# Optimization experiments

Hardware: AMD Instinct MI355X
Metric: run time of the kernel (lower is better)

The kernel has to match this reference:

```python
import jax, jax.numpy as jnp
import numpy as np
from jax import lax

B, T_IN, N, C_IN = 64, 12, 716, 2
RC = DC = 32      # residual / dilation channels
SC = 8            # skip channels
EC = 512          # end channels
OUT = 12
DIMS = 40
DAYS = 288
TOD = 288
TOPK = 100
DILS = [1, 2, 1, 2, 1, 2, 1, 2]  # blocks=4, layers=2
L = len(DILS)


def setup_inputs() -> dict:
    key = jax.random.key(0)
    ks = iter(jax.random.split(key, 64))
    n = lambda shape, s=0.1: jax.random.normal(next(ks), shape, jnp.float32) * s
    return dict(
        history_data=jax.random.uniform(next(ks), (B, T_IN, N, C_IN), jnp.float32),
        alpha=jnp.float32(-5.0),
        nodevec_p1=n((DAYS, DIMS), 1.0),
        nodevec_p2=n((N, DIMS), 1.0),
        nodevec_p3=n((N, DIMS), 1.0),
        nodevec_pk=n((DIMS, DIMS, DIMS), 1.0),
        pivweight=n((N, N), 1.0),
        start_W=n((RC, 1)), start_b=n((RC,)),
        starta_W=n((1, 1)), starta_b=n((1,)),
        filter_W=n((L, DC, RC, 1, 2)), filter_b=n((L, DC)),
        gate_W=n((L, DC, RC, 1, 2)), gate_b=n((L, DC)),
        skip_W=n((L, SC, DC)), skip_b=n((L, SC)),
        gconv_W=n((L, RC, 3 * DC)), gconv_b=n((L, RC)),
        pgconv_W=n((L, RC, 3 * RC)), pgconv_b=n((L, RC)),
        bn_gamma=jnp.ones((L, RC), jnp.float32),
        bn_beta=jnp.zeros((L, RC), jnp.float32),
        end1_W=n((EC, SC * 52)), end1_b=n((EC,)),
        end2_W=n((OUT, EC)), end2_b=n((OUT,)),
    )


def _conv1x1(x, W, b):  # x [B,C,N,T], W [O,C]
    return jnp.einsum('bcnt,oc->bont', x, W) + b[None, :, None, None]


def _gcn(x, A, W, b):
    # diffusion order 2 over one support; A [B,N,N] or [N,N]
    sub = 'bcvt,bwv->bcwt' if A.ndim == 3 else 'bcvt,wv->bcwt'
    x1 = jnp.einsum(sub, x, A)
    x2 = jnp.einsum(sub, x1, A)
    return _conv1x1(jnp.concatenate([x, x1, x2], axis=1), W, b)


def _forward(history_data, alpha, nodevec_p1, nodevec_p2, nodevec_p3, nodevec_pk,
             pivweight, start_W, start_b, starta_W, starta_b,
             filter_W, filter_b, gate_W, gate_b, skip_W, skip_b,
             gconv_W, gconv_b, pgconv_W, pgconv_b, bn_gamma, bn_beta,
             end1_W, end1_b, end2_W, end2_b):
    inputs = jnp.transpose(history_data[..., 0:1], (0, 3, 2, 1))  # [B,1,N,T]
    inputs = jnp.pad(inputs, ((0, 0), (0, 0), (0, 0), (1, 0)))    # T -> 13 = receptive field
    ind = (history_data[:, -1, 0, 1] * TOD).astype(jnp.int32) % DAYS

    x = _conv1x1(inputs, start_W, start_b)      # [B,RC,N,13]
    x_a = _conv1x1(inputs, starta_W, starta_b)  # [B,1,N,13]

    # dynamic adjacency (dgconstruct)
    adp = jnp.einsum('ai,ijk->ajk', nodevec_p1[ind], nodevec_pk)
    adp = jnp.einsum('bj,ajk->abk', nodevec_p2, adp)
    adp = jnp.einsum('ck,abk->abc', nodevec_p3, adp)
    adj = jax.nn.softmax(jax.nn.relu(adp), axis=2)  # [B,N,N]

    # pivotal adjacency (pivotalconstruct) with top-k node mask
    xs = x_a[:, 0].sum(0)                   # [N,T]
    y = xs.sum(1)[None, :]                  # [1,N]
    adjp = (xs[:, :-1] @ xs[:, 1:].T) / y   # [N,N]
    adjp = adjp * pivweight
    score = adjp.sum(0) + adjp.sum(1)
    _, idx = lax.top_k(score, TOPK)
    mask = jnp.zeros((N,), bool).at[idx].set(True)
    adj_p = jax.nn.softmax(jax.nn.relu(adjp * mask[:, None] * mask[None, :]), axis=1)  # [N,N]

    a_s = jax.nn.sigmoid(alpha)
    dn = ('NCHW', 'OIHW', 'NCHW')
    skip = None
    for i, d in enumerate(DILS):
        residual = x
        filt = jnp.tanh(
            lax.conv_general_dilated(residual, filter_W[i], (1, 1), 'VALID',
                                     rhs_dilation=(1, d), dimension_numbers=dn)
            + filter_b[i][None, :, None, None])
        gate = jax.nn.sigmoid(
            lax.conv_general_dilated(residual, gate_W[i], (1, 1), 'VALID',
                                     rhs_dilation=(1, d), dimension_numbers=dn)
            + gate_b[i][None, :, None, None])
        xg = _gcn(filt * gate, adj, gconv_W[i], gconv_b[i])  # [B,RC,N,T-d]
        # pgcn: diffusion on residual, then causal temporal crop by dilation
        xa = _gcn(residual, adj_p, pgconv_W[i], pgconv_b[i])[..., : residual.shape[3] - d]
        x = a_s * xa + (1.0 - a_s) * xg
        x = x + residual[..., -x.shape[3]:]
        s = _conv1x1(x, skip_W[i], skip_b[i])  # [B,SC,N,Ti]
        s = jnp.transpose(s, (0, 1, 3, 2)).reshape(s.shape[0], -1, s.shape[2], 1)  # [B,SC*Ti,N,1]
        skip = s if skip is None else jnp.concatenate([s, skip], axis=1)
        # BatchNorm2d, train-mode batch stats, fresh affine
        mu = x.mean(axis=(0, 2, 3), keepdims=True)
        var = x.var(axis=(0, 2, 3), keepdims=True)
        x = ((x - mu) / jnp.sqrt(var + 1e-5)) * bn_gamma[i][None, :, None, None] \
            + bn_beta[i][None, :, None, None]

    out = jax.nn.relu(skip)                         # [B,SC*52,N,1]
    out = jax.nn.relu(_conv1x1(out, end1_W, end1_b))
    out = _conv1x1(out, end2_W, end2_b)             # [B,OUT,N,1]
    return out


def reference(history_data, alpha, nodevec_p1, nodevec_p2, nodevec_p3, nodevec_pk,
              pivweight, start_W, start_b, starta_W, starta_b,
              filter_W, filter_b, gate_W, gate_b, skip_W, skip_b,
              gconv_W, gconv_b, pgconv_W, pgconv_b, bn_gamma, bn_beta,
              end1_W, end1_b, end2_W, end2_b):
    return _forward(history_data, alpha, nodevec_p1, nodevec_p2, nodevec_p3, nodevec_pk,
                    pivweight, start_W, start_b, starta_W, starta_b,
                    filter_W, filter_b, gate_W, gate_b, skip_W, skip_b,
                    gconv_W, gconv_b, pgconv_W, pgconv_b, bn_gamma, bn_beta,
                    end1_W, end1_b, end2_W, end2_b)
```

## Files before the change

### kernel.cpp

```cpp
#include <hip/hip_runtime.h>
#include <math.h>

#define NN 716
#define NSQ (716*716)
#define MAXG 9216
#define FPAD 70
typedef unsigned short bfu;
typedef __attribute__((ext_vector_type(8))) __bf16 bf16x8;
typedef __attribute__((ext_vector_type(4))) float f32x4;

__device__ __forceinline__ float b2f(bfu u){ union{unsigned int i; float f;} x; x.i = ((unsigned int)u)<<16; return x.f; }
__device__ __forceinline__ bfu f2b(float f){ union{float fv; unsigned int i;} x; x.fv = f; unsigned int r = (x.i + 0x7fffu + ((x.i>>16)&1u)) >> 16; return (bfu)r; }
__device__ __forceinline__ float sigmoidf_(float x){ return 1.f/(1.f+expf(-x)); }

__device__ __forceinline__ float fexp_(float x){
#if __has_builtin(__builtin_amdgcn_exp2f)
  return __builtin_amdgcn_exp2f(x * 1.44269504088896340736f);
#else
  return __expf(x);
#endif
}
__device__ __forceinline__ float frcp_(float x){
#if __has_builtin(__builtin_amdgcn_rcpf)
  return __builtin_amdgcn_rcpf(x);
#else
  return 1.f/x;
#endif
}
__device__ __forceinline__ float fsig_(float x){ return frcp_(1.f + fexp_(-x)); }
__device__ __forceinline__ float ftanh_(float x){
  float xc = fminf(fmaxf(x, -30.f), 30.f);
  float e = fexp_(-2.f*xc);
  return (1.f - e) * frcp_(1.f + e);
}


__global__ void k_ind(const float* __restrict__ hist, int* __restrict__ ind){
  int b = threadIdx.x; if (b >= 64) return;
  float v = hist[((b*12+11)*NN + 0)*2 + 1];
  ind[b] = ((int)(v*288.0f)) % 288;
}

__global__ void k_dg1(const float* __restrict__ p1, const float* __restrict__ pk,
                      const int* __restrict__ ind, float* __restrict__ tmp1){
  int b = blockIdx.x;
  __shared__ float p1s[40];
  if (threadIdx.x < 40) p1s[threadIdx.x] = p1[ind[b]*40 + threadIdx.x];
  __syncthreads();
  for (int jk = threadIdx.x; jk < 1600; jk += 256){
    float acc = 0.f;
    for (int i = 0; i < 40; ++i) acc += p1s[i]*pk[i*1600 + jk];
    tmp1[b*1600 + jk] = acc;
  }
}

__global__ void k_dg2(const float* __restrict__ p2, const float* __restrict__ tmp1,
                      float* __restrict__ tmp2){
  int b = blockIdx.y;
  __shared__ float ts[1600];
  for (int i = threadIdx.x; i < 1600; i += 256) ts[i] = tmp1[b*1600+i];
  __syncthreads();
  int idx = blockIdx.x*256 + threadIdx.x;
  if (idx >= NN*40) return;
  int n = idx/40, k = idx%40;
  float acc = 0.f;
  for (int j = 0; j < 40; ++j) acc += p2[n*40+j]*ts[j*40+k];
  tmp2[(long)b*NN*40 + idx] = acc;
}

__global__ void k_p3t(const float* __restrict__ p3, float* __restrict__ p3t){
  int v = blockIdx.x*256 + threadIdx.x; if (v >= NN) return;
  for (int k = 0; k < 40; ++k) p3t[k*NN + v] = p3[v*40 + k];
}

__global__ __launch_bounds__(256) void k_adjrow4s(const float* __restrict__ p3t,
    const float* __restrict__ tmp2, unsigned int* __restrict__ topA,
    int* __restrict__ cntA)
{
  int b = blockIdx.y, w0 = blockIdx.x*4, tid = threadIdx.x;
  int wave = tid >> 6, lane = tid & 63;
  __shared__ float t2s[4][40];
  __shared__ float buf[4][720];
  __shared__ float wred[4][4];
  __shared__ float rstat[4];
  __shared__ int pc[4][12];
  for (int i = tid; i < 160; i += 256){
    int r = i/40, k = i%40; int w = w0 + r;
    t2s[r][k] = (w < NN) ? tmp2[((long)b*NN + w)*40 + k] : 0.f;
  }
  __syncthreads();
  float lmax[4] = {0,0,0,0};
  for (int q = 0; q < 3; ++q){
    int v = tid + q*256;
    if (v < NN){
      float a[4] = {0,0,0,0};
      #pragma unroll 8
      for (int k = 0; k < 40; ++k){
        float pv = p3t[k*NN + v];
        #pragma unroll
        for (int r = 0; r < 4; ++r) a[r] += t2s[r][k]*pv;
      }
      #pragma unroll
      for (int r = 0; r < 4; ++r){
        float val = fmaxf(a[r], 0.f);
        buf[r][v] = val;
        lmax[r] = fmaxf(lmax[r], val);
      }
    }
  }
  #pragma unroll
  for (int r = 0; r < 4; ++r){
    float m = lmax[r];
    for (int s = 32; s > 0; s >>= 1) m = fmaxf(m, __shfl_xor(m, s, 64));
    if (lane == 0) wred[r][wave] = m;
  }
  __syncthreads();
  if (tid < 4) rstat[tid] = fmaxf(fmaxf(wred[tid][0], wred[tid][1]), fmaxf(wred[tid][2], wred[tid][3]));
  __syncthreads();
  float lsum[4] = {0,0,0,0};
  for (int q = 0; q < 3; ++q){
    int v = tid + q*256;
    if (v < NN){
      #pragma unroll
      for (int r = 0; r < 4; ++r){
        float e = fexp_(buf[r][v] - rstat[r]);
        buf[r][v] = e;
        lsum[r] += e;
      }
    }
  }
  __syncthreads();
  #pragma unroll
  for (int r = 0; r < 4; ++r){
    float s = lsum[r];
    for (int k = 32; k > 0; k >>= 1) s += __shfl_xor(s, k, 64);
    if (lane == 0) wred[r][wave] = s;
  }
  __syncthreads();
  if (tid < 4) rstat[tid] = frcp_(wred[tid][0] + wred[tid][1] + wred[tid][2] + wred[tid][3]);
  __syncthreads();
  for (int q = 0; q < 3; ++q){
    int v = tid + q*256;
    #pragma unroll
    for (int r = 0; r < 4; ++r){
      float p = (v < NN) ? buf[r][v]*rstat[r] : 0.f;
      unsigned long long m = __ballot(p >= 1e-7f);
      if (lane == 0) pc[r][q*4+wave] = __popcll(m);
    }
  }
  __syncthreads();
  for (int q = 0; q < 3; ++q){
    int v = tid + q*256;
    #pragma unroll
    for (int r = 0; r < 4; ++r){
      float p = (v < NN) ? buf[r][v]*rstat[r] : 0.f;
      bool qual = (p >= 1e-7f);
      unsigned long long m = __ballot(qual);
      int w = w0 + r;
      if (qual && w < NN){
        int base = 0, me = q*4+wave;
        for (int s = 0; s < me; ++s) base += pc[r][s];
        unsigned long long below = (lane == 0) ? 0ull : (m << (64-lane) >> (64-lane));
        int pos = base + __popcll(below);
        if (pos < 16)
          topA[((long)b*NN + w)*16 + pos] = (((unsigned)v)<<16) | (unsigned)f2b(p);
      }
    }
  }
  __syncthreads();
  if (tid < 4){
    int w = w0 + tid;
    if (w < NN){
      int tot = 0;
      for (int s = 0; s < 12; ++s) tot += pc[tid][s];
      cntA[(long)b*NN + w] = (tot < 16) ? tot : 16;
    }
  }
}

__global__ __launch_bounds__(256) void k_zgather(const bfu* __restrict__ Xg,
    const unsigned int* __restrict__ topA, const int* __restrict__ cntA,
    bfu* __restrict__ Zg, int M, long sx, long sz)
{
  __shared__ bfu rows[4][720];
  int b = blockIdx.y;
  int tid = threadIdx.x, wave = tid >> 6, lane = tid & 63;
  int m = blockIdx.x*4 + wave;
  if (m < M){
    const bfu* xr = Xg + (long)b*sx + (long)m*NN;
    #pragma unroll
    for (int q = 0; q < 12; ++q){
      int v = lane + q*64;
      if (v < NN) rows[wave][v] = xr[v];
    }
  }
  __syncthreads();
  if (m >= M) return;
  bfu* zr = Zg + (long)b*sz + (long)m*NN;
  const unsigned int* ta = topA + (long)b*NN*16;
  const int* ca = cntA + (long)b*NN;
  #pragma unroll
  for (int q = 0; q < 12; ++q){
    int w = lane + q*64;
    if (w < NN){
      int cnt = ca[w];
      const unsigned int* lst = ta + (long)w*16;
      float acc = 0.f;
      for (int j = 0; j < cnt; ++j){
        unsigned int e = lst[j];
        acc += b2f((bfu)(e & 0xffffu)) * b2f(rows[wave][e >> 16]);
      }
      zr[w] = f2b(acc);
    }
  }
}

__global__ void k_xs(const float* __restrict__ hist, const float* __restrict__ saW,
                     const float* __restrict__ sab, float* __restrict__ xs, float* __restrict__ y){
  int n = blockIdx.x, b = threadIdx.x;
  float w = saW[0], bb = sab[0];
  float ytot = 0.f;
  for (int t = 0; t < 13; ++t){
    float inp = (t == 0) ? 0.f : hist[((b*12 + (t-1))*NN + n)*2];
    float s = inp;
    for (int off = 32; off > 0; off >>= 1) s += __shfl_down(s, off, 64);
    if (b == 0){ float val = w*s + 64.f*bb; xs[n*13+t] = val; ytot += val; }
  }
  if (b == 0) y[n] = ytot;
}

__global__ void k_adjp(const float* __restrict__ xs, const float* __restrict__ y,
                       const float* __restrict__ piv, float* __restrict__ adjp){
  int i = blockIdx.y;
  __shared__ float xi[13];
  if (threadIdx.x < 13) xi[threadIdx.x] = xs[i*13+threadIdx.x];
  __syncthreads();
  int j = blockIdx.x*256 + threadIdx.x;
  if (j >= NN) return;
  float acc = 0.f;
  #pragma unroll
  for (int t = 0; t < 12; ++t) acc += xi[t]*xs[j*13+t+1];
  adjp[(long)i*NN+j] = acc / y[j] * piv[(long)i*NN+j];
}

__global__ void k_score(const float* __restrict__ adjp, float* __restrict__ score){
  int n = blockIdx.x, tid = threadIdx.x;
  float s = 0.f;
  for (int i = tid; i < NN; i += 256) s += adjp[(long)i*NN+n] + adjp[(long)n*NN+i];
  __shared__ float red[256];
  red[tid] = s; __syncthreads();
  for (int k = 128; k > 0; k >>= 1){ if (tid < k) red[tid] += red[tid+k]; __syncthreads(); }
  if (tid == 0) score[n] = red[0];
}

__global__ void k_topk(const float* __restrict__ score, int* __restrict__ mask){
  __shared__ float v[1024];
  __shared__ int ix[1024];
  int tid = threadIdx.x;
  for (int t = tid; t < 1024; t += 256){ v[t] = (t < NN) ? score[t] : -INFINITY; ix[t] = t; }
  __syncthreads();
  for (int k = 2; k <= 1024; k <<= 1){
    for (int j = k >> 1; j > 0; j >>= 1){
      for (int t = tid; t < 1024; t += 256){
        int l = t ^ j;
        if (l > t){
          bool up = ((t & k) == 0);
          bool g = (v[t] > v[l]) || (v[t] == v[l] && ix[t] < ix[l]);
          if (up ? !g : g){
            float tv = v[t]; v[t] = v[l]; v[l] = tv;
            int ti = ix[t]; ix[t] = ix[l]; ix[l] = ti;
          }
        }
      }
      __syncthreads();
    }
  }
  for (int t = tid; t < NN; t += 256) mask[t] = 0;
  __syncthreads();
  if (tid < 100) mask[ix[tid]] = 1;
}

__global__ void k_pivprep(const float* __restrict__ adjp, const int* __restrict__ mask,
                          int* __restrict__ idxk, int* __restrict__ rankv,
                          float* __restrict__ uvec, float* __restrict__ ApkT){
  __shared__ int sidx[100];
  int tid = threadIdx.x;
  if (tid == 0){
    int c = 0;
    for (int i = 0; i < NN; ++i){
      if (mask[i] && c < 100){ sidx[c] = i; idxk[c] = i; rankv[i] = c; ++c; }
      else rankv[i] = -1;
    }
  }
  __syncthreads();
  if (tid < 100){
    int i = sidx[tid];
    const float* row = adjp + (long)i*NN;
    float mx = 0.f;
    for (int k = 0; k < 100; ++k) mx = fmaxf(mx, row[sidx[k]]);
    float sum = 616.f * fexp_(-mx);
    for (int k = 0; k < 100; ++k) sum += fexp_(fmaxf(row[sidx[k]], 0.f) - mx);
    float inv = 1.f/sum;
    uvec[tid] = fexp_(-mx)*inv;
    for (int k = 0; k < 100; ++k)
      ApkT[k*100 + tid] = fexp_(fmaxf(row[sidx[k]], 0.f) - mx)*inv;
  }
}

__global__ void k_init_x(const float* __restrict__ hist, const float* __restrict__ sW,
                         const float* __restrict__ sb, bfu* __restrict__ x){
  int n = blockIdx.x*256 + threadIdx.x; if (n >= NN) return;
  int t = blockIdx.y, b = blockIdx.z;
  float inp = (t == 0) ? 0.f : hist[((b*12 + (t-1))*NN + n)*2];
  #pragma unroll
  for (int c = 0; c < 32; ++c)
    x[((long)(b*32+c)*13 + t)*NN + n] = f2b(sW[c]*inp + sb[c]);
}

__global__ void k_bnid(float* __restrict__ bnp){
  int c = threadIdx.x; if (c >= 32) return;
  bnp[c*2] = 1.f; bnp[c*2+1] = 0.f;
}

__global__ void k_bnfold(const float* __restrict__ fW, const float* __restrict__ fb,
                         const float* __restrict__ gW, const float* __restrict__ gb,
                         const float* __restrict__ bnp, bfu* __restrict__ Wcat,
                         float* __restrict__ bcat){
  int tid = threadIdx.x;
  for (int i = tid; i < 4096; i += 256){
    int row = i >> 6, k = i & 63;
    int o = row >> 1, isg = row & 1;
    int tap = k >> 5, c = k & 31;
    const float* W = isg ? gW : fW;
    Wcat[i] = f2b(W[(o*32+c)*2 + tap] * bnp[c*2]);
  }
  if (tid < 64){
    int o = tid >> 1, isg = tid & 1;
    const float* W = isg ? gW : fW;
    const float* B = isg ? gb : fb;
    float s = B[o];
    for (int c = 0; c < 32; ++c)
      s += (W[(o*32+c)*2] + W[(o*32+c)*2+1]) * bnp[c*2+1];
    bcat[tid] = s;
  }
}

__global__ void k_e1perm(const float* __restrict__ W, bfu* __restrict__ Wb){
  int i = blockIdx.x*256 + threadIdx.x;
  if (i >= 512*416) return;
  int e = i/416, kp = i%416;
  const int off2[9] = {0,96,176,248,304,352,384,408,416};
  const int soff[8] = {320,240,168,112,64,32,8,0};
  const int tpl[8]  = {12,10,9,7,6,4,3,1};
  int L = 0;
  #pragma unroll
  for (int q = 0; q < 8; ++q) if (kp >= off2[q+1]) L = q+1;
  int r = kp - off2[L]; int t = r>>3, sc = r&7;
  int k = soff[L] + sc*tpl[L] + t;
  Wb[e*416+kp] = f2b(W[e*416+k]);
}

#define LDST 44

__global__ __launch_bounds__(256) void gemm_mfma(const bfu* __restrict__ Xg,
    const bfu* __restrict__ Ag, bfu* __restrict__ Cg,
    int M, int K, long sx, long sa, long sc,
    const float* __restrict__ bias, int relu_out, int Trow, int Tcomp)
{
  int bx = gridDim.x, by = gridDim.y, nb = gridDim.z;
  int bX = blockIdx.x, bY = blockIdx.y, bZ = blockIdx.z;
  int bpb = bx*by, total = bpb*nb;
  if ((total & 7) == 0 && (nb & 7) == 0){
    int L = bX + bx*(bY + by*bZ);
    int xcd = L & 7, slot = L >> 3;
    bZ = xcd*(nb >> 3) + slot/bpb;
    int inner = slot % bpb;
    bX = inner % bx; bY = inner / bx;
  }
  const bfu* X = Xg + (long)bZ*sx;
  const bfu* A = Ag + (long)bZ*sa;
  bfu*       C = Cg + (long)bZ*sc;
  int m0 = bY*128, n0 = bX*128;
  __shared__ bfu Xs[128*LDST];
  __shared__ bfu As[128*LDST];
  int tid = threadIdx.x;
  int wave = tid >> 6, lane = tid & 63;
  int wm = (wave >> 1)*64, wn = (wave & 1)*64;
  int lr = lane & 15, lg = lane >> 4;
  f32x4 acc[4][4] = {};
  int ldr = tid >> 1, ldk = (tid & 1)*16;
  int mg = m0 + ldr, ng = n0 + ldr;
  int mrow = (Trow == Tcomp) ? mg : (mg/Tcomp)*Trow + (mg%Tcomp);
  const bfu* xrow = X + (long)mrow*K;
  const bfu* arow = A + (long)ng*K;
  for (int k0 = 0; k0 < K; k0 += 32){
    int kk = k0 + ldk;
    ushort4 z4 = {0,0,0,0};
    ushort4 x0=z4,x1=z4,x2=z4,x3=z4, a0=z4,a1=z4,a2=z4,a3=z4;
    if (mg < M){
      if (kk + 16 <= K){
        const ushort4* s = (const ushort4*)(xrow + kk);
        x0=s[0]; x1=s[1]; x2=s[2]; x3=s[3];
      } else {
        bfu tv[16];
        #pragma unroll
        for (int j=0;j<16;++j) tv[j] = (kk+j < K) ? xrow[kk+j] : (bfu)0;
        const ushort4* s = (const ushort4*)tv;
        x0=s[0]; x1=s[1]; x2=s[2]; x3=s[3];
      }
    }
    if (ng < NN){
      if (kk + 16 <= K){
        const ushort4* s = (const ushort4*)(arow + kk);
        a0=s[0]; a1=s[1]; a2=s[2]; a3=s[3];
      } else {
        bfu tv[16];
        #pragma unroll
        for (int j=0;j<16;++j) tv[j] = (kk+j < K) ? arow[kk+j] : (bfu)0;
        const ushort4* s = (const ushort4*)tv;
        a0=s[0]; a1=s[1]; a2=s[2]; a3=s[3];
      }
    }
    ushort4* xd = (ushort4*)&Xs[ldr*LDST + ldk];
    xd[0]=x0; xd[1]=x1; xd[2]=x2; xd[3]=x3;
    ushort4* ad = (ushort4*)&As[ldr*LDST + ldk];
    ad[0]=a0; ad[1]=a1; ad[2]=a2; ad[3]=a3;
    __syncthreads();
    bf16x8 af[4], bfr[4];
    #pragma unroll
    for (int i=0;i<4;++i){
      af[i]  = *(const bf16x8*)&Xs[(wm + i*16 + lr)*LDST + lg*8];
      bfr[i] = *(const bf16x8*)&As[(wn + i*16 + lr)*LDST + lg*8];
    }
    #pragma unroll
    for (int i=0;i<4;++i)
      #pragma unroll
      for (int j=0;j<4;++j)
        acc[i][j] = __builtin_amdgcn_mfma_f32_16x16x32_bf16(af[i], bfr[j], acc[i][j], 0,0,0);
    __syncthreads();
  }
  #pragma unroll
  for (int i=0;i<4;++i){
    #pragma unroll
    for (int r=0;r<4;++r){
      int m = m0 + wm + i*16 + lg*4 + r;
      if (m >= M) continue;
      float bv = bias ? bias[m] : 0.f;
      #pragma unroll
      for (int j=0;j<4;++j){
        int n = n0 + wn + j*16 + lr;
        if (n < NN){
          float v = acc[i][j][r] + bv;
          if (relu_out) v = fmaxf(v, 0.f);
          C[(long)m*NN + n] = f2b(v);
        }
      }
    }
  }
}

__global__ __launch_bounds__(256) void k_fg_mfma(const bfu* __restrict__ x,
    const bfu* __restrict__ Wcat, const float* __restrict__ bcat,
    bfu* __restrict__ fg, int T, int Tp, int d)
{
  __shared__ bfu Bsh[128*FPAD];
  __shared__ bfu Ash[64*FPAD];
  __shared__ float bsh[64];
  int tid = threadIdx.x;
  int n0 = blockIdx.x*128, t = blockIdx.y, b = blockIdx.z;
  for (int i = tid; i < 4096; i += 256){
    int row = i >> 6, k = i & 63;
    Ash[row*FPAD + k] = Wcat[i];
  }
  if (tid < 64) bsh[tid] = bcat[tid];
  #pragma unroll
  for (int i = 0; i < 8; ++i){
    int idx = tid + i*256;
    int n4 = (idx & 31)*4;
    int cc = idx >> 5;
    int c = cc & 31, tap = cc >> 5;
    long base = ((long)(b*32+c)*T + t + (tap ? d : 0))*NN + n0 + n4;
    ushort4 v = {0,0,0,0};
    if (n0 + n4 < NN) v = *(const ushort4*)(x + base);
    Bsh[(n4+0)*FPAD + cc] = v.x;
    Bsh[(n4+1)*FPAD + cc] = v.y;
    Bsh[(n4+2)*FPAD + cc] = v.z;
    Bsh[(n4+3)*FPAD + cc] = v.w;
  }
  __syncthreads();
  int wave = tid >> 6, lane = tid & 63;
  int lr = lane & 15, lg = lane >> 4;
  int rowbase = wave*16;
  bf16x8 a0 = *(const bf16x8*)&Ash[(rowbase+lr)*FPAD + lg*8];
  bf16x8 a1 = *(const bf16x8*)&Ash[(rowbase+lr)*FPAD + 32 + lg*8];
  float bf0 = bsh[rowbase + lg*4 + 0];
  float bg0 = bsh[rowbase + lg*4 + 1];
  float bf1 = bsh[rowbase + lg*4 + 2];
  float bg1 = bsh[rowbase + lg*4 + 3];
  int o0 = (rowbase >> 1) + lg*2;
  #pragma unroll
  for (int nt = 0; nt < 8; ++nt){
    bf16x8 b0 = *(const bf16x8*)&Bsh[(nt*16+lr)*FPAD + lg*8];
    bf16x8 b1 = *(const bf16x8*)&Bsh[(nt*16+lr)*FPAD + 32 + lg*8];
    f32x4 acc = {};
    acc = __builtin_amdgcn_mfma_f32_16x16x32_bf16(a0, b0, acc, 0,0,0);
    acc = __builtin_amdgcn_mfma_f32_16x16x32_bf16(a1, b1, acc, 0,0,0);
    int n = n0 + nt*16 + lr;
    if (n < NN){
      float f0 = acc[0] + bf0, g0 = acc[1] + bg0;
      float f1 = acc[2] + bf1, g1 = acc[3] + bg1;
      fg[((long)(b*32+o0)*Tp + t)*NN + n]   = f2b(ftanh_(f0)*fsig_(g0));
      fg[((long)(b*32+o0+1)*Tp + t)*NN + n] = f2b(ftanh_(f1)*fsig_(g1));
    }
  }
}

__global__ __launch_bounds__(256) void k_pgdiff1c(const bfu* __restrict__ X,
    float* __restrict__ U, bfu* __restrict__ Yk,
    const int* __restrict__ idxk, const float* __restrict__ uvec,
    const float* __restrict__ ApkT, const float* __restrict__ bnp,
    int M, int Trow, int Tcomp)
{
  __shared__ float xks[4][100];
  int tid = threadIdx.x;
  int g = tid >> 6, lane = tid & 63;
  int m = blockIdx.x*4 + g;
  bool act = (m < M);
  float s = 0.f, sk = 0.f;
  if (act){
    int mrow = (m/Tcomp)*Trow + (m%Tcomp);
    const bfu* xr = X + (long)mrow*NN;
    #pragma unroll
    for (int q = 0; q < 12; ++q){
      int v = lane + q*64;
      if (v < NN) s += b2f(xr[v]);
    }
    for (int o = 32; o; o >>= 1) s += __shfl_xor(s, o, 64);
    #pragma unroll
    for (int q = 0; q < 2; ++q){
      int k = lane + q*64;
      if (k < 100){
        float v = b2f(xr[idxk[k]]);
        xks[g][k] = v;
        sk += v;
      }
    }
    for (int o = 32; o; o >>= 1) sk += __shfl_xor(sk, o, 64);
  }
  __syncthreads();
  if (!act) return;
  int c = (m / Tcomp) & 31;
  float sb = bnp[c*2], bb = bnp[c*2+1];
  if (lane == 0) U[m] = sb*(s*(1.f/716.f)) + bb;
  #pragma unroll
  for (int q = 0; q < 2; ++q){
    int r = lane + q*64;
    if (r < 100){
      float acc = uvec[r]*(s - sk);
      for (int k = 0; k < 100; ++k) acc += ApkT[k*100 + r]*xks[g][k];
      Yk[(long)m*100 + r] = f2b(sb*acc + bb);
    }
  }
}

__global__ __launch_bounds__(256) void k_pgdiff2c(const float* __restrict__ U1,
    const bfu* __restrict__ Y1k, float* __restrict__ U2, bfu* __restrict__ Y2k,
    const float* __restrict__ uvec, const float* __restrict__ ApkT, int M)
{
  __shared__ float yks[4][100];
  int tid = threadIdx.x;
  int g = tid >> 6, lane = tid & 63;
  int m = blockIdx.x*4 + g;
  bool act = (m < M);
  float sumY = 0.f;
  if (act){
    const bfu* yr = Y1k + (long)m*100;
    #pragma unroll
    for (int q = 0; q < 2; ++q){
      int k = lane + q*64;
      if (k < 100){
        float v = b2f(yr[k]);
        yks[g][k] = v;
        sumY += v;
      }
    }
    for (int o = 32; o; o >>= 1) sumY += __shfl_xor(sumY, o, 64);
  }
  __syncthreads();
  if (!act) return;
  float base = 616.f*U1[m];
  if (lane == 0) U2[m] = (base + sumY)*(1.f/716.f);
  #pragma unroll
  for (int q = 0; q < 2; ++q){
    int r = lane + q*64;
    if (r < 100){
      float acc = uvec[r]*base;
      for (int k = 0; k < 100; ++k) acc += ApkT[k*100 + r]*yks[g][k];
      Y2k[(long)m*100 + r] = f2b(acc);
    }
  }
}

__global__ __launch_bounds__(256) void k_ymix(const float* __restrict__ U1,
    const float* __restrict__ U2, const bfu* __restrict__ Y1k, const bfu* __restrict__ Y2k,
    const float* __restrict__ pWl, float* __restrict__ V12, float* __restrict__ M12, int Tp)
{
  int t = blockIdx.x, b = blockIdx.y, tid = threadIdx.x;
  __shared__ float w1t[1024], w2t[1024];
  __shared__ float y1s[3200], y2s[3200];
  __shared__ float u1s[32], u2s[32];
  for (int i = tid; i < 1024; i += 256){
    int o = i & 31, c = i >> 5;
    w1t[c*32+o] = pWl[o*96+32+c];
    w2t[c*32+o] = pWl[o*96+64+c];
  }
  for (int i = tid; i < 3200; i += 256){
    int c = i/100, r = i - c*100;
    long m = (long)(b*32+c)*Tp + t;
    y1s[i] = b2f(Y1k[m*100 + r]);
    y2s[i] = b2f(Y2k[m*100 + r]);
  }
  if (tid < 32){
    long m = (long)(b*32+tid)*Tp + t;
    u1s[tid] = U1[m]; u2s[tid] = U2[m];
  }
  __syncthreads();
  for (int i = tid; i < 3200; i += 256){
    int r = i >> 5, o = i & 31;
    float acc = 0.f;
    #pragma unroll 8
    for (int c = 0; c < 32; ++c)
      acc += w1t[c*32+o]*y1s[c*100+r] + w2t[c*32+o]*y2s[c*100+r];
    M12[((long)(b*Tp+t)*100 + r)*32 + o] = acc;
  }
  if (tid < 32){
    float acc = 0.f;
    #pragma unroll 8
    for (int c = 0; c < 32; ++c)
      acc += w1t[c*32+tid]*u1s[c] + w2t[c*32+tid]*u2s[c];
    V12[(long)(b*Tp+t)*32 + tid] = acc;
  }
}


__global__ __launch_bounds__(256) void k_xgmix1n(bfu* __restrict__ F,
    const bfu* __restrict__ z1, const bfu* __restrict__ z2,
    const float* __restrict__ Wl, const float* __restrict__ bl,
    const float* __restrict__ alpha, int Tp)
{
  __shared__ float w0t[1024], w1t[1024], w2t[1024], bb[32];
  for (int i = threadIdx.x; i < 1024; i += 256){
    int o = i & 31, c = i >> 5;
    w0t[c*32+o] = Wl[o*96+c];
    w1t[c*32+o] = Wl[o*96+32+c];
    w2t[c*32+o] = Wl[o*96+64+c];
  }
  if (threadIdx.x < 32) bb[threadIdx.x] = bl[threadIdx.x];
  __syncthreads();
  int n = blockIdx.x*256 + threadIdx.x; if (n >= NN) return;
  int t = blockIdx.y, b = blockIdx.z;
  float acc[32];
  #pragma unroll
  for (int o = 0; o < 32; ++o) acc[o] = bb[o];
  const float4* w04 = (const float4*)w0t;
  const float4* w14 = (const float4*)w1t;
  const float4* w24 = (const float4*)w2t;
  #pragma unroll 4
  for (int c = 0; c < 32; ++c){
    long off = ((long)(b*32+c)*Tp + t)*NN + n;
    float f0 = b2f(F[off]);
    float a0 = b2f(z1[off]);
    float b0 = b2f(z2[off]);
    #pragma unroll
    for (int o4 = 0; o4 < 8; ++o4){
      float4 w0v = w04[c*8+o4], w1v = w14[c*8+o4], w2v = w24[c*8+o4];
      acc[o4*4+0] += w0v.x*f0 + w1v.x*a0 + w2v.x*b0;
      acc[o4*4+1] += w0v.y*f0 + w1v.y*a0 + w2v.y*b0;
      acc[o4*4+2] += w0v.z*f0 + w1v.z*a0 + w2v.z*b0;
      acc[o4*4+3] += w0v.w*f0 + w1v.w*a0 + w2v.w*b0;
    }
  }
  float oma = 1.f - sigmoidf_(alpha[0]);
  #pragma unroll
  for (int o = 0; o < 32; ++o)
    F[((long)(b*32+o)*Tp + t)*NN + n] = f2b(oma*acc[o]);
}

__global__ __launch_bounds__(256) void k_combine3nb(const bfu* __restrict__ x,
    bfu* __restrict__ F, const int* __restrict__ rankv,
    const float* __restrict__ M12, const float* __restrict__ V12,
    const float* __restrict__ pWl, const float* __restrict__ pbl,
    const float* __restrict__ skWl, const float* __restrict__ skbl,
    const float* __restrict__ alpha, const float* __restrict__ bnp,
    bfu* __restrict__ skipP, float* __restrict__ bnred,
    int T, int Tp, int d, int off2)
{
  __shared__ float w0t[1024];
  __shared__ float Ms[101*33];
  __shared__ float swt[256], bnl[64], pbs[32], sb8[8];
  int t = blockIdx.y, b = blockIdx.z, tid = threadIdx.x;
  for (int i = tid; i < 1024; i += 256){
    int o = i & 31, c = i >> 5;
    w0t[c*32+o] = pWl[o*96+c];
  }
  for (int i = tid; i < 3333; i += 256){
    int r = i/33, o = i - r*33;
    if (o < 32)
      Ms[r*33+o] = (r < 100) ? M12[((long)(b*Tp+t)*100 + r)*32 + o]
                             : V12[(long)(b*Tp+t)*32 + o];
  }
  swt[tid] = skWl[tid];
  if (tid < 64) bnl[tid] = bnp[tid];
  if (tid < 32) pbs[tid] = pbl[tid];
  if (tid < 8)  sb8[tid] = skbl[tid];
  __syncthreads();
  int n = blockIdx.x*256 + tid;
  bool act = (n < NN);
  float acc[32];
  #pragma unroll
  for (int o = 0; o < 32; ++o) acc[o] = pbs[o];
  const float4* w04 = (const float4*)w0t;
  if (act){
    #pragma unroll 4
    for (int c = 0; c < 32; ++c){
      float sc = bnl[c*2], bc = bnl[c*2+1];
      float x0 = b2f(x[((long)(b*32+c)*T + t)*NN + n])*sc + bc;
      #pragma unroll
      for (int o4 = 0; o4 < 8; ++o4){
        float4 w = w04[c*8+o4];
        acc[o4*4+0] += w.x*x0;
        acc[o4*4+1] += w.y*x0;
        acc[o4*4+2] += w.z*x0;
        acc[o4*4+3] += w.w*x0;
      }
    }
  }
  int ra = act ? rankv[n] : -1;
  int sel = (ra < 0) ? 100 : ra;
  float a_s = sigmoidf_(alpha[0]);
  #pragma unroll
  for (int o = 0; o < 32; ++o){
    float v = 0.f;
    if (act){
      float scb = bnl[o*2], bcb = bnl[o*2+1];
      long oidx = ((long)(b*32+o)*Tp + t)*NN + n;
      float gv  = b2f(F[oidx]);
      float res = b2f(x[((long)(b*32+o)*T + t + d)*NN + n])*scb + bcb;
      v = a_s*(acc[o] + Ms[sel*33+o]) + gv + res;
      F[oidx] = f2b(v);
    }
    acc[o] = v;
  }
  {
    int wave = tid >> 6;
    int gid = ((blockIdx.x + gridDim.x*(blockIdx.y + gridDim.y*blockIdx.z)) << 2) + wave;
    #pragma unroll
    for (int o = 0; o < 32; ++o){
      float v = acc[o], vq = v*v;
      for (int s = 32; s; s >>= 1){
        v  += __shfl_xor(v,  s, 64);
        vq += __shfl_xor(vq, s, 64);
      }
      if ((tid & 63) == 0){
        bnred[((long)o*MAXG + gid)*2]     = v;
        bnred[((long)o*MAXG + gid)*2 + 1] = vq;
      }
    }
  }
  if (!act) return;
  const float4* sw4 = (const float4*)swt;
  #pragma unroll
  for (int sc2 = 0; sc2 < 8; ++sc2){
    float s0 = sb8[sc2];
    #pragma unroll
    for (int c4 = 0; c4 < 8; ++c4){
      float4 w = sw4[sc2*8 + c4];
      s0 += w.x*acc[c4*4] + w.y*acc[c4*4+1] + w.z*acc[c4*4+2] + w.w*acc[c4*4+3];
    }
    skipP[((long)b*416 + off2 + t*8 + sc2)*NN + n] = f2b(fmaxf(s0, 0.f));
  }
}

__global__ void k_bn2v2(const float* __restrict__ red, const float* __restrict__ gamma,
                        const float* __restrict__ beta, float* __restrict__ bnp,
                        int layer, int Tp, int ngroups){
  int c = blockIdx.x, tid = threadIdx.x;
  float s = 0.f, s2 = 0.f;
  for (int g = tid; g < ngroups; g += 256){
    s  += red[((long)c*MAXG + g)*2];
    s2 += red[((long)c*MAXG + g)*2 + 1];
  }
  __shared__ float rs[256], rs2[256];
  rs[tid] = s; rs2[tid] = s2; __syncthreads();
  for (int k = 128; k > 0; k >>= 1){
    if (tid < k){ rs[tid] += rs[tid+k]; rs2[tid] += rs2[tid+k]; }
    __syncthreads();
  }
  if (tid == 0){
    float cnt = 64.f*Tp*716.f;
    float mu = rs[0]/cnt, var = rs2[0]/cnt - mu*mu;
    float rstd = rsqrtf(var + 1e-5f);
    float ga = gamma[layer*32+c], be = beta[layer*32+c];
    bnp[c*2] = rstd*ga; bnp[c*2+1] = be - mu*rstd*ga;
  }
}


__global__ __launch_bounds__(256) void k_sktr(const bfu* __restrict__ SP, bfu* __restrict__ ST){
  __shared__ bfu tile[64][66];
  int b = blockIdx.z;
  int n0 = blockIdx.x*64, k0 = blockIdx.y*64;
  int tid = threadIdx.x;
  int tr = tid >> 6, tc = tid & 63;
  #pragma unroll
  for (int p = 0; p < 16; ++p){
    int k = k0 + p*4 + tr, n = n0 + tc;
    tile[p*4+tr][tc] = (k < 416 && n < NN) ? SP[((long)b*416 + k)*NN + n] : (bfu)0;
  }
  __syncthreads();
  #pragma unroll
  for (int p = 0; p < 16; ++p){
    int n = n0 + p*4 + tr, k = k0 + tc;
    if (n < NN && k < 416) ST[((long)b*NN + n)*416 + k] = tile[tc][p*4+tr];
  }
}

__global__ __launch_bounds__(256) void k_end2(const bfu* __restrict__ H,
    const float* __restrict__ W2, const float* __restrict__ b2, float* __restrict__ out)
{
  __shared__ float w[12*512];
  for (int i = threadIdx.x; i < 6144; i += 256) w[i] = W2[i];
  __syncthreads();
  int n = blockIdx.x*256 + threadIdx.x; if (n >= NN) return;
  int b = blockIdx.y;
  float acc[12];
  #pragma unroll
  for (int o = 0; o < 12; ++o) acc[o] = b2[o];
  for (int e = 0; e < 512; ++e){
    float h = b2f(H[((long)b*512+e)*NN + n]);
    #pragma unroll
    for (int o = 0; o < 12; ++o) acc[o] += w[o*512+e]*h;
  }
  #pragma unroll
  for (int o = 0; o < 12; ++o) out[((long)b*12+o)*NN + n] = acc[o];
}


extern "C" void kernel_launch(void* const* d_in, const int* in_sizes, int n_in,
                              void* d_out, int out_size, void* d_ws, size_t ws_size,
                              hipStream_t stream)
{
  const float* hist = (const float*)d_in[0];
  const float* alpha = (const float*)d_in[1];
  const float* p1  = (const float*)d_in[2];
  const float* p2  = (const float*)d_in[3];
  const float* p3  = (const float*)d_in[4];
  const float* pk  = (const float*)d_in[5];
  const float* piv = (const float*)d_in[6];
  const float* sW  = (const float*)d_in[7];
  const float* sb  = (const float*)d_in[8];
  const float* saW = (const float*)d_in[9];
  const float* sab = (const float*)d_in[10];
  const float* fW  = (const float*)d_in[11];
  const float* fb  = (const float*)d_in[12];
  const float* gW  = (const float*)d_in[13];
  const float* gb  = (const float*)d_in[14];
  const float* skW = (const float*)d_in[15];
  const float* skb = (const float*)d_in[16];
  const float* gcW = (const float*)d_in[17];
  const float* gcb = (const float*)d_in[18];
  const float* pgW = (const float*)d_in[19];
  const float* pgb = (const float*)d_in[20];
  const float* bng = (const float*)d_in[21];
  const float* bnb = (const float*)d_in[22];
  const float* e1W = (const float*)d_in[23];
  const float* e1b = (const float*)d_in[24];
  const float* e2W = (const float*)d_in[25];
  const float* e2b = (const float*)d_in[26];
  float* out = (float*)d_out;

  char* base = (char*)d_ws;
  size_t off = 0;
  auto alloc = [&](size_t bytes)->char*{
    char* r = base + off;
    off = (off + bytes + 255) & ~(size_t)255;
    return r;
  };
  const size_t SZ12 = 64UL*32*12*716*2;
  const size_t SZ13 = 64UL*32*13*716*2;
  bfu*   t1    = (bfu*)  alloc(SZ12);
  bfu*   t2    = (bfu*)  alloc(SZ12);
  bfu*   P     = (bfu*)  alloc(SZ13);
  bfu*   Q     = (bfu*)  alloc(SZ12);
  bfu*   skipP = (bfu*)  alloc(64UL*416*716*2);
  bfu*   skipT = (bfu*)  alloc(64UL*716*416*2);
  float* adjp  = (float*)alloc((size_t)NSQ*4);
  float* tmp1  = (float*)alloc(64UL*1600*4);
  float* tmp2  = (float*)alloc(64UL*716*40*4);
  float* p3t   = (float*)alloc(40UL*716*4);
  bfu*   e1Wb  = (bfu*)  alloc(512UL*416*2);
  unsigned int* topA = (unsigned int*)alloc(64UL*NN*16*4);
  int*   cntA  = (int*)  alloc(64UL*NN*4);
  bfu*   Wcat  = (bfu*)  alloc(4096UL*2);
  float* bcat  = (float*)alloc(64UL*4);
  float* xs    = (float*)alloc(716UL*13*4);
  float* yv    = (float*)alloc(716UL*4);
  float* score = (float*)alloc(716UL*4);
  float* bnred = (float*)alloc(32UL*MAXG*2*4);
  float* bnp   = (float*)alloc(64UL*4);
  float* bnpid = (float*)alloc(64UL*4);
  float* uvec  = (float*)alloc(100UL*4);
  float* ApkT  = (float*)alloc(100UL*100*4);
  int*   ind   = (int*)  alloc(64UL*4);
  int*   mask  = (int*)  alloc(716UL*4);
  int*   idxk  = (int*)  alloc(100UL*4);
  int*   rankv = (int*)  alloc(716UL*4);

  char* t1c = (char*)t1;
  float* U1  = (float*)(t1c);
  float* U2  = (float*)(t1c +   98304);
  float* V12 = (float*)(t1c + 2*98304);
  float* M12 = (float*)(t1c + 3*98304);
  bfu*   Y1k = (bfu*)  (t1c + 3*98304 + 9830400);
  bfu*   Y2k = (bfu*)  (t1c + 3*98304 + 9830400 + 4915200);

  bfu* hidden = t1;

  k_ind<<<1,64,0,stream>>>(hist, ind);
  k_dg1<<<64,256,0,stream>>>(p1, pk, ind, tmp1);
  k_dg2<<<dim3(112,64),256,0,stream>>>(p2, tmp1, tmp2);
  k_p3t<<<3,256,0,stream>>>(p3, p3t);
  k_adjrow4s<<<dim3(179,64),256,0,stream>>>(p3t, tmp2, topA, cntA);
  k_xs<<<716,64,0,stream>>>(hist, saW, sab, xs, yv);
  k_adjp<<<dim3(3,716),256,0,stream>>>(xs, yv, piv, adjp);
  k_score<<<716,256,0,stream>>>(adjp, score);
  k_topk<<<1,256,0,stream>>>(score, mask);
  k_pivprep<<<1,256,0,stream>>>(adjp, mask, idxk, rankv, uvec, ApkT);
  k_init_x<<<dim3(3,13,64),256,0,stream>>>(hist, sW, sb, P);
  k_e1perm<<<(512*416+255)/256,256,0,stream>>>(e1W, e1Wb);
  k_bnid<<<1,64,0,stream>>>(bnpid);

  int T = 13;
  bfu* x = P;
  bfu* F = Q;
  static const int off2_[8] = {0,96,176,248,304,352,384,408};
  for (int i = 0; i < 8; ++i){
    int d = (i & 1) ? 2 : 1;
    int Tp = T - d;
    const float* bnin = (i == 0) ? bnpid : bnp;
    dim3 g3(3, Tp, 64);
    k_bnfold<<<1,256,0,stream>>>(fW + i*2048, fb + i*32, gW + i*2048, gb + i*32,
        bnin, Wcat, bcat);
    k_fg_mfma<<<dim3(6,Tp,64),256,0,stream>>>(x, Wcat, bcat, F, T, Tp, d);
    int M1 = 32*Tp; long sx1 = (long)M1*NN;
    dim3 gz((M1+3)/4, 64);
    k_zgather<<<gz,256,0,stream>>>(F,  topA, cntA, t1, M1, sx1, sx1);
    k_zgather<<<gz,256,0,stream>>>(t1, topA, cntA, t2, M1, sx1, sx1);
    k_xgmix1n<<<g3,256,0,stream>>>(F, t1, t2, gcW + i*3072, gcb + i*32, alpha, Tp);
    int M2 = 64*32*Tp;
    k_pgdiff1c<<<M2/4,256,0,stream>>>(x, U1, Y1k, idxk, uvec, ApkT, bnin, M2, T, Tp);
    k_pgdiff2c<<<M2/4,256,0,stream>>>(U1, Y1k, U2, Y2k, uvec, ApkT, M2);
    k_ymix<<<dim3(Tp,64),256,0,stream>>>(U1, U2, Y1k, Y2k, pgW + i*3072, V12, M12, Tp);
    k_combine3nb<<<g3,256,0,stream>>>(x, F, rankv, M12, V12, pgW + i*3072, pgb + i*32,
        skW + i*256, skb + i*8, alpha, bnin, skipP, bnred, T, Tp, d, off2_[i]);
    int ngroups = 3*Tp*64*4;
    k_bn2v2<<<32,256,0,stream>>>(bnred, bng, bnb, bnp, i, Tp, ngroups);
    bfu* tmp = x; x = F; F = tmp;
    T = Tp;
  }
  k_sktr<<<dim3(12,7,64),256,0,stream>>>(skipP, skipT);
  gemm_mfma<<<dim3(6,4,64),256,0,stream>>>(e1Wb, skipT, hidden, 512, 416,
      0L, 416L*716, 512L*716, e1b, 1, 1, 1);
  k_end2<<<dim3(3,64),256,0,stream>>>(hidden, e2W, e2b, out);
}
```

Measured before the change: 2.913 ms.

## Fuse two sparse diffusion gathers into one kernel; remap blocks across XCDs

The two back-to-back top-k sparse gather kernels are merged into one. The first-hop result row is kept in shared memory and reused for the second hop, so t1 no longer has to be re-read from global memory and one launch disappears per layer. The fg and combine kernels also remap the linear block index so that blocks for the same batch land on the same XCD, aiming for better L2 locality. This adds shared-memory use per block and some index arithmetic.

```diff
diff --git a/kernel.cpp b/kernel.cpp
--- a/kernel.cpp
+++ b/kernel.cpp
@@ -178,11 +178,12 @@
   }
 }
 
-__global__ __launch_bounds__(256) void k_zgather(const bfu* __restrict__ Xg,
+__global__ __launch_bounds__(256) void k_zgather2(const bfu* __restrict__ Xg,
     const unsigned int* __restrict__ topA, const int* __restrict__ cntA,
-    bfu* __restrict__ Zg, int M, long sx, long sz)
+    bfu* __restrict__ Z1g, bfu* __restrict__ Z2g, int M, long sx)
 {
   __shared__ bfu rows[4][720];
+  __shared__ bfu zrow[4][720];
   int b = blockIdx.y;
   int tid = threadIdx.x, wave = tid >> 6, lane = tid & 63;
   int m = blockIdx.x*4 + wave;
@@ -195,10 +196,30 @@
     }
   }
   __syncthreads();
-  if (m >= M) return;
-  bfu* zr = Zg + (long)b*sz + (long)m*NN;
   const unsigned int* ta = topA + (long)b*NN*16;
   const int* ca = cntA + (long)b*NN;
+  if (m < M){
+    bfu* zr = Z1g + (long)b*sx + (long)m*NN;
+    #pragma unroll
+    for (int q = 0; q < 12; ++q){
+      int w = lane + q*64;
+      if (w < NN){
+        int cnt = ca[w];
+        const unsigned int* lst = ta + (long)w*16;
+        float acc = 0.f;
+        for (int j = 0; j < cnt; ++j){
+          unsigned int e = lst[j];
+          acc += b2f((bfu)(e & 0xffffu)) * b2f(rows[wave][e >> 16]);
+        }
+        bfu zv = f2b(acc);
+        zr[w] = zv;
+        zrow[wave][w] = zv;
+      }
+    }
+  }
+  __syncthreads();
+  if (m >= M) return;
+  bfu* z2r = Z2g + (long)b*sx + (long)m*NN;
   #pragma unroll
   for (int q = 0; q < 12; ++q){
     int w = lane + q*64;
@@ -208,9 +229,9 @@
       float acc = 0.f;
       for (int j = 0; j < cnt; ++j){
         unsigned int e = lst[j];
-        acc += b2f((bfu)(e & 0xffffu)) * b2f(rows[wave][e >> 16]);
-      }
-      zr[w] = f2b(acc);
+        acc += b2f((bfu)(e & 0xffffu)) * b2f(zrow[wave][e >> 16]);
+      }
+      z2r[w] = f2b(acc);
     }
   }
 }
@@ -467,7 +488,13 @@
   __shared__ bfu Ash[64*FPAD];
   __shared__ float bsh[64];
   int tid = threadIdx.x;
-  int n0 = blockIdx.x*128, t = blockIdx.y, b = blockIdx.z;
+  int tot6 = 6*Tp;
+  int L = blockIdx.x + 6*(blockIdx.y + Tp*blockIdx.z);
+  int xcd = L & 7, slot = L >> 3;
+  int b = xcd + ((slot/tot6) << 3);
+  int r6 = slot - (slot/tot6)*tot6;
+  int t = r6/6, nb6 = r6 - (r6/6)*6;
+  int n0 = nb6*128;
   for (int i = tid; i < 4096; i += 256){
     int row = i >> 6, k = i & 63;
     Ash[row*FPAD + k] = Wcat[i];
@@ -698,7 +725,13 @@
   __shared__ float w0t[1024];
   __shared__ float Ms[101*33];
   __shared__ float swt[256], bnl[64], pbs[32], sb8[8];
-  int t = blockIdx.y, b = blockIdx.z, tid = threadIdx.x;
+  int tid = threadIdx.x;
+  int tot3 = 3*Tp;
+  int L = blockIdx.x + 3*(blockIdx.y + Tp*blockIdx.z);
+  int xcd = L & 7, slot = L >> 3;
+  int b = xcd + ((slot/tot3) << 3);
+  int r3 = slot - (slot/tot3)*tot3;
+  int t = r3/3, bx3 = r3 - (r3/3)*3;
   for (int i = tid; i < 1024; i += 256){
     int o = i & 31, c = i >> 5;
     w0t[c*32+o] = pWl[o*96+c];
@@ -714,7 +747,7 @@
   if (tid < 32) pbs[tid] = pbl[tid];
   if (tid < 8)  sb8[tid] = skbl[tid];
   __syncthreads();
-  int n = blockIdx.x*256 + tid;
+  int n = bx3*256 + tid;
   bool act = (n < NN);
   float acc[32];
   #pragma unroll
@@ -954,8 +987,7 @@
     k_fg_mfma<<<dim3(6,Tp,64),256,0,stream>>>(x, Wcat, bcat, F, T, Tp, d);
     int M1 = 32*Tp; long sx1 = (long)M1*NN;
     dim3 gz((M1+3)/4, 64);
-    k_zgather<<<gz,256,0,stream>>>(F,  topA, cntA, t1, M1, sx1, sx1);
-    k_zgather<<<gz,256,0,stream>>>(t1, topA, cntA, t2, M1, sx1, sx1);
+    k_zgather2<<<gz,256,0,stream>>>(F, topA, cntA, t1, t2, M1, sx1);
     k_xgmix1n<<<g3,256,0,stream>>>(F, t1, t2, gcW + i*3072, gcb + i*32, alpha, Tp);
     int M2 = 64*32*Tp;
     k_pgdiff1c<<<M2/4,256,0,stream>>>(x, U1, Y1k, idxk, uvec, ApkT, bnin, M2, T, Tp);
```

Result: faster. 2.851 ms (-2.1%).
